# Performance work log

Hardware: AMD Instinct MI355X
Metric: run time of the kernel (lower is better)

The kernel has to match this reference:

```python
import jax, jax.numpy as jnp
import numpy as np

BLOCK = 128  # fp8 block-quant block size (block_size = [128, 128])


def _dequant(w, s):
    # w: [E, O, I] fp8-simulated values; s: [E, O, I//BLOCK] per-block scales
    # (scale_inv already repeat_interleaved along the out dim by the module).
    E, O, I = w.shape
    nb = s.shape[-1]
    bs = I // nb
    return (w.reshape(E, O, nb, bs) * s[..., None]).reshape(E, O, I)


def setup_inputs() -> dict:
    key = jax.random.key(0)
    ks = jax.random.split(key, 8)
    B, S, H, I, E = 1, 512, 2048, 768, 16
    return {
        "hidden_states": jax.random.normal(ks[0], (B, S, H), jnp.float32),
        "gate_w": jax.random.normal(ks[1], (E, H), jnp.float32) * 0.02,
        "w1": jax.random.normal(ks[2], (E, I, H), jnp.float32),
        "w1_scale": jax.random.uniform(ks[3], (E, I, H // BLOCK), jnp.float32, 0.005, 0.02),
        "w3": jax.random.normal(ks[4], (E, I, H), jnp.float32),
        "w3_scale": jax.random.uniform(ks[5], (E, I, H // BLOCK), jnp.float32, 0.005, 0.02),
        "w2": jax.random.normal(ks[6], (E, H, I), jnp.float32),
        "w2_scale": jax.random.uniform(ks[7], (E, H, I // BLOCK), jnp.float32, 0.005, 0.02),
        "top_k": 2,
    }


def reference(hidden_states, gate_w, w1, w1_scale, w3, w3_scale, w2, w2_scale, top_k):
    B, S, H = hidden_states.shape
    x = hidden_states.reshape(-1, H)           # [T, H]
    T = x.shape[0]
    E = gate_w.shape[0]

    # Router: sigmoid scores, top-k, sum-normalization (norm_topk_prob=False)
    router_logits = x @ gate_w.T               # [T, E]
    scores = jax.nn.sigmoid(router_logits.astype(jnp.float32))
    top_w, top_i = jax.lax.top_k(scores, top_k)
    top_w = top_w / jnp.sum(top_w, axis=-1, keepdims=True)

    # Dense combine matrix [T, E] (top-k sparse in the real kernel)
    combine = jnp.zeros((T, E), x.dtype).at[jnp.arange(T)[:, None], top_i].add(
        top_w.astype(x.dtype))

    # Inline block dequantization of fp8 weights
    w1d = _dequant(w1, w1_scale)               # [E, I, H]
    w3d = _dequant(w3, w3_scale)               # [E, I, H]
    w2d = _dequant(w2, w2_scale)               # [E, H, I]

    # SwiGLU expert MLPs (grouped GEMM expressed densely over experts)
    g = jnp.einsum('th,eih->eti', x, w1d)      # gate proj
    u = jnp.einsum('th,eih->eti', x, w3d)      # up proj
    a = jax.nn.silu(g) * u                     # [E, T, I]
    expert_out = jnp.einsum('eti,ehi->eth', a, w2d)  # down proj [E, T, H]

    y = jnp.einsum('te,eth->th', combine, expert_out)
    return y.reshape(B, S, H)
```

## Files before the change

kernel.cpp:

```cpp
#include <hip/hip_runtime.h>
#include <math.h>

#define H 2048
#define II 768
#define TT 512
#define EE 16
#define BK 64

typedef float f32x4 __attribute__((ext_vector_type(4)));
typedef short s16x8 __attribute__((ext_vector_type(8)));
typedef unsigned short u16;
typedef u16 u16x4 __attribute__((ext_vector_type(4)));
typedef u16 u16x8 __attribute__((ext_vector_type(8)));

__device__ __forceinline__ u16 f2bf(float f) {
  unsigned int u = __float_as_uint(f);
  u += 0x7fffu + ((u >> 16) & 1u);
  return (u16)(u >> 16);
}

__global__ void router_kernel(const float* __restrict__ x, const float* __restrict__ gw,
                              int* __restrict__ counts, int* __restrict__ topi,
                              float* __restrict__ topw, int* __restrict__ pos) {
  int t = blockIdx.x;
  int tid = threadIdx.x;
  int wave = tid >> 6, lane = tid & 63;
  __shared__ float logits[EE];
  const float* xt = x + (size_t)t * H;
  for (int e = wave * 4; e < wave * 4 + 4; ++e) {
    const float* ge = gw + (size_t)e * H;
    float p = 0.f;
    for (int h = lane * 4; h < H; h += 64 * 4) {
      f32x4 xv = *(const f32x4*)(xt + h);
      f32x4 gv = *(const f32x4*)(ge + h);
      p += xv[0]*gv[0] + xv[1]*gv[1] + xv[2]*gv[2] + xv[3]*gv[3];
    }
    #pragma unroll
    for (int off = 32; off > 0; off >>= 1) p += __shfl_down(p, off);
    if (lane == 0) logits[e] = p;
  }
  __syncthreads();
  if (tid == 0) {
    float s[EE];
    #pragma unroll
    for (int e = 0; e < EE; ++e) s[e] = 1.f / (1.f + expf(-logits[e]));
    int i0 = 0;
    for (int e = 1; e < EE; ++e) if (s[e] > s[i0]) i0 = e;
    int i1 = -1;
    for (int e = 0; e < EE; ++e) {
      if (e == i0) continue;
      if (i1 < 0 || s[e] > s[i1]) i1 = e;
    }
    float w0 = s[i0], w1v = s[i1];
    float inv = 1.f / (w0 + w1v);
    w0 *= inv; w1v *= inv;
    topi[t*2+0] = i0; topi[t*2+1] = i1;
    topw[t*2+0] = w0; topw[t*2+1] = w1v;
    pos[t*2+0] = atomicAdd(&counts[i0], 1);
    pos[t*2+1] = atomicAdd(&counts[i1], 1);
  }
}

__global__ void prefix_kernel(const int* __restrict__ counts, int* __restrict__ base) {
  int s = 0;
  for (int e = 0; e < EE; ++e) { base[e] = s; s += counts[e]; }
  base[EE] = s;
}

__global__ void gather_kernel(const float* __restrict__ x, const int* __restrict__ topi,
                              const float* __restrict__ topw, const int* __restrict__ pos,
                              const int* __restrict__ base, u16* __restrict__ Xg,
                              int* __restrict__ tok_of, float* __restrict__ wt_of) {
  int t = blockIdx.x, slot = blockIdx.y;
  int e = topi[t*2 + slot];
  int row = base[e] + pos[t*2 + slot];
  if (threadIdx.x == 0) { tok_of[row] = t; wt_of[row] = topw[t*2 + slot]; }
  const float* xt = x + (size_t)t * H;
  u16* dst = Xg + (size_t)row * H;
  int h = threadIdx.x * 8;
  f32x4 v0 = *(const f32x4*)(xt + h);
  f32x4 v1 = *(const f32x4*)(xt + h + 4);
  u16x8 o;
  o[0]=f2bf(v0[0]); o[1]=f2bf(v0[1]); o[2]=f2bf(v0[2]); o[3]=f2bf(v0[3]);
  o[4]=f2bf(v1[0]); o[5]=f2bf(v1[1]); o[6]=f2bf(v1[2]); o[7]=f2bf(v1[3]);
  *(u16x8*)(dst + h) = o;
}

__global__ __launch_bounds__(256, 8) void gemm1_kernel(
    const u16* __restrict__ Xg,
    const float* __restrict__ w1, const float* __restrict__ w1s,
    const float* __restrict__ w3, const float* __restrict__ w3s,
    const int* __restrict__ counts, const int* __restrict__ base,
    float* __restrict__ slab) {
  const int bx = blockIdx.x;
  const int nc = bx >> 2, kc = bx & 3;
  const int e = blockIdx.y;
  const int cnt = counts[e];
  if (cnt == 0) return;
  const int n0 = nc * 16;
  const int k0 = kc * 512;
  const int b0 = base[e];
  const int tid = threadIdx.x;
  const int lane = tid & 63;
  const int w = tid >> 6;

  __shared__ __align__(16) u16 As[64 * 64];
  __shared__ __align__(16) u16 Bs[2][16 * 64];

  const int rA = tid >> 3;
  const int cA = (tid & 7) << 3;
  const int cAs = cA ^ ((rA & 7) << 3);
  const int isB3 = tid >> 7;
  const int rB = (tid & 127) >> 3;
  const int cBs = cA ^ ((rB & 7) << 3);
  const float* wsrc = (isB3 ? w3 : w1) + (size_t)(e * II + n0 + rB) * H + k0 + cA;
  const float* ssrc = (isB3 ? w3s : w1s) + (size_t)(e * II + n0 + rB) * (H / 128) + kc * 4;
  u16* bdst = &Bs[isB3][rB * 64 + cBs];

  const int arow = w * 16 + (lane & 15);
  const int acol0 = (lane >> 4) << 3;
  const int brow = lane & 15;
  const int aswz = (arow & 7) << 3;
  const int bswz = (brow & 7) << 3;

  float* outG = slab + ((size_t)kc) * ((size_t)1024 * II);
  float* outU = slab + ((size_t)(4 + kc)) * ((size_t)1024 * II);

  const int nmt = (cnt + 63) >> 6;
  for (int mt = 0; mt < nmt; ++mt) {
    const u16* asrc = Xg + (size_t)(b0 + mt * 64 + rA) * H + k0 + cA;
    f32x4 accg = {}, accu = {};
    s16x8 a0, a1; f32x4 bv0, bv1; float sc;
    a0 = *(const s16x8*)(asrc);
    a1 = *(const s16x8*)(asrc + (size_t)32 * H);
    bv0 = *(const f32x4*)(wsrc);
    bv1 = *(const f32x4*)(wsrc + 4);
    sc = ssrc[0];
    {
      *(s16x8*)(As + rA * 64 + cAs) = a0;
      *(s16x8*)(As + (rA + 32) * 64 + cAs) = a1;
      u16x8 ob;
      ob[0]=f2bf(bv0[0]*sc); ob[1]=f2bf(bv0[1]*sc); ob[2]=f2bf(bv0[2]*sc); ob[3]=f2bf(bv0[3]*sc);
      ob[4]=f2bf(bv1[0]*sc); ob[5]=f2bf(bv1[1]*sc); ob[6]=f2bf(bv1[2]*sc); ob[7]=f2bf(bv1[3]*sc);
      *(u16x8*)bdst = ob;
    }
    __syncthreads();
    for (int t = 0; t < 512 / BK; ++t) {
      const bool notlast = (t + 1 < 512 / BK);
      if (notlast) {
        const int k1 = (t + 1) * BK;
        a0 = *(const s16x8*)(asrc + k1);
        a1 = *(const s16x8*)(asrc + (size_t)32 * H + k1);
        bv0 = *(const f32x4*)(wsrc + k1);
        bv1 = *(const f32x4*)(wsrc + k1 + 4);
        sc = ssrc[k1 >> 7];
      }
      #pragma unroll
      for (int ks = 0; ks < 2; ++ks) {
        const int ac = ks * 32 + acol0;
        s16x8 af  = *(const s16x8*)(As + arow * 64 + (ac ^ aswz));
        const int bix = brow * 64 + (ac ^ bswz);
        s16x8 b1f = *(const s16x8*)(Bs[0] + bix);
        s16x8 b3f = *(const s16x8*)(Bs[1] + bix);
        accg = __builtin_amdgcn_mfma_f32_16x16x32_bf16(af, b1f, accg, 0, 0, 0);
        accu = __builtin_amdgcn_mfma_f32_16x16x32_bf16(af, b3f, accu, 0, 0, 0);
      }
      __syncthreads();
      if (notlast) {
        *(s16x8*)(As + rA * 64 + cAs) = a0;
        *(s16x8*)(As + (rA + 32) * 64 + cAs) = a1;
        u16x8 ob;
        ob[0]=f2bf(bv0[0]*sc); ob[1]=f2bf(bv0[1]*sc); ob[2]=f2bf(bv0[2]*sc); ob[3]=f2bf(bv0[3]*sc);
        ob[4]=f2bf(bv1[0]*sc); ob[5]=f2bf(bv1[1]*sc); ob[6]=f2bf(bv1[2]*sc); ob[7]=f2bf(bv1[3]*sc);
        *(u16x8*)bdst = ob;
      }
      __syncthreads();
    }
    const int col = n0 + (lane & 15);
    #pragma unroll
    for (int r4 = 0; r4 < 4; ++r4) {
      int mrow = mt * 64 + w * 16 + ((lane >> 4) << 2) + r4;
      if (mrow < cnt) {
        outG[(size_t)(b0 + mrow) * II + col] = accg[r4];
        outU[(size_t)(b0 + mrow) * II + col] = accu[r4];
      }
    }
  }
}

__global__ void silu_kernel(const float* __restrict__ slab, u16* __restrict__ Ag) {
  const size_t i = ((size_t)blockIdx.x * 256 + threadIdx.x) * 4;
  const float* G = slab;
  const float* U = slab + (size_t)4 * 1024 * II;
  f32x4 g = {}, u = {};
  #pragma unroll
  for (int kc = 0; kc < 4; ++kc) {
    g += *(const f32x4*)(G + (size_t)kc * 1024 * II + i);
    u += *(const f32x4*)(U + (size_t)kc * 1024 * II + i);
  }
  u16x4 o;
  #pragma unroll
  for (int j = 0; j < 4; ++j) {
    float a = g[j] / (1.f + expf(-g[j])) * u[j];
    o[j] = f2bf(a);
  }
  *(u16x4*)(Ag + i) = o;
}

__global__ __launch_bounds__(256, 8) void gemm2_kernel(
    const u16* __restrict__ Ag,
    const float* __restrict__ w2, const float* __restrict__ w2s,
    const int* __restrict__ counts, const int* __restrict__ base,
    const int* __restrict__ tok_of, const float* __restrict__ wt_of,
    float* __restrict__ y) {
  const int bx = blockIdx.x;
  const int nc = bx >> 1, kc = bx & 1;
  const int e = blockIdx.y;
  const int cnt = counts[e];
  if (cnt == 0) return;
  const int n0 = nc * 32;
  const int k0 = kc * 384;
  const int b0 = base[e];
  const int tid = threadIdx.x;
  const int lane = tid & 63;
  const int w = tid >> 6;

  __shared__ __align__(16) u16 As[64 * 64];
  __shared__ __align__(16) u16 Bs[32 * 64];

  const int rA = tid >> 3;
  const int cA = (tid & 7) << 3;
  const int cAs = cA ^ ((rA & 7) << 3);
  const int rB = tid >> 3;
  const int cBs = cA ^ ((rB & 7) << 3);
  const float* wsrc = w2 + (size_t)(e * H + n0 + rB) * II + k0 + cA;
  const float* ssrc = w2s + (size_t)(e * H + n0 + rB) * (II / 128) + kc * 3;
  u16* bdst = &Bs[rB * 64 + cBs];

  const int arow = w * 16 + (lane & 15);
  const int acol0 = (lane >> 4) << 3;
  const int brow = lane & 15;
  const int aswz = (arow & 7) << 3;

  const int nmt = (cnt + 63) >> 6;
  for (int mt = 0; mt < nmt; ++mt) {
    const u16* asrc = Ag + (size_t)(b0 + mt * 64 + rA) * II + k0 + cA;
    f32x4 acc0 = {}, acc1 = {};
    s16x8 a0, a1; f32x4 bv0, bv1; float sc;
    a0 = *(const s16x8*)(asrc);
    a1 = *(const s16x8*)(asrc + (size_t)32 * II);
    bv0 = *(const f32x4*)(wsrc);
    bv1 = *(const f32x4*)(wsrc + 4);
    sc = ssrc[0];
    {
      *(s16x8*)(As + rA * 64 + cAs) = a0;
      *(s16x8*)(As + (rA + 32) * 64 + cAs) = a1;
      u16x8 ob;
      ob[0]=f2bf(bv0[0]*sc); ob[1]=f2bf(bv0[1]*sc); ob[2]=f2bf(bv0[2]*sc); ob[3]=f2bf(bv0[3]*sc);
      ob[4]=f2bf(bv1[0]*sc); ob[5]=f2bf(bv1[1]*sc); ob[6]=f2bf(bv1[2]*sc); ob[7]=f2bf(bv1[3]*sc);
      *(u16x8*)bdst = ob;
    }
    __syncthreads();
    for (int t = 0; t < 384 / BK; ++t) {
      const bool notlast = (t + 1 < 384 / BK);
      if (notlast) {
        const int k1 = (t + 1) * BK;
        a0 = *(const s16x8*)(asrc + k1);
        a1 = *(const s16x8*)(asrc + (size_t)32 * II + k1);
        bv0 = *(const f32x4*)(wsrc + k1);
        bv1 = *(const f32x4*)(wsrc + k1 + 4);
        sc = ssrc[k1 >> 7];
      }
      #pragma unroll
      for (int ks = 0; ks < 2; ++ks) {
        const int ac = ks * 32 + acol0;
        s16x8 af  = *(const s16x8*)(As + arow * 64 + (ac ^ aswz));
        s16x8 b0f = *(const s16x8*)(Bs + brow * 64 + (ac ^ ((brow & 7) << 3)));
        const int br1 = brow + 16;
        s16x8 b1f = *(const s16x8*)(Bs + br1 * 64 + (ac ^ ((br1 & 7) << 3)));
        acc0 = __builtin_amdgcn_mfma_f32_16x16x32_bf16(af, b0f, acc0, 0, 0, 0);
        acc1 = __builtin_amdgcn_mfma_f32_16x16x32_bf16(af, b1f, acc1, 0, 0, 0);
      }
      __syncthreads();
      if (notlast) {
        *(s16x8*)(As + rA * 64 + cAs) = a0;
        *(s16x8*)(As + (rA + 32) * 64 + cAs) = a1;
        u16x8 ob;
        ob[0]=f2bf(bv0[0]*sc); ob[1]=f2bf(bv0[1]*sc); ob[2]=f2bf(bv0[2]*sc); ob[3]=f2bf(bv0[3]*sc);
        ob[4]=f2bf(bv1[0]*sc); ob[5]=f2bf(bv1[1]*sc); ob[6]=f2bf(bv1[2]*sc); ob[7]=f2bf(bv1[3]*sc);
        *(u16x8*)bdst = ob;
      }
      __syncthreads();
    }
    #pragma unroll
    for (int r4 = 0; r4 < 4; ++r4) {
      int mrow = mt * 64 + w * 16 + ((lane >> 4) << 2) + r4;
      if (mrow < cnt) {
        int grow = b0 + mrow;
        int t = tok_of[grow];
        float wt = wt_of[grow];
        atomicAdd(y + (size_t)t * H + n0 + (lane & 15), acc0[r4] * wt);
        atomicAdd(y + (size_t)t * H + n0 + 16 + (lane & 15), acc1[r4] * wt);
      }
    }
  }
}

extern "C" void kernel_launch(void* const* d_in, const int* in_sizes, int n_in,
                              void* d_out, int out_size, void* d_ws, size_t ws_size,
                              hipStream_t stream) {
  const float* x   = (const float*)d_in[0];
  const float* gw  = (const float*)d_in[1];
  const float* w1  = (const float*)d_in[2];
  const float* w1s = (const float*)d_in[3];
  const float* w3  = (const float*)d_in[4];
  const float* w3s = (const float*)d_in[5];
  const float* w2  = (const float*)d_in[6];
  const float* w2s = (const float*)d_in[7];
  float* y = (float*)d_out;

  char* ws = (char*)d_ws;
  int*   counts = (int*)(ws + 0);
  int*   basep  = (int*)(ws + 64);
  int*   topi   = (int*)(ws + 256);
  float* topw   = (float*)(ws + 256 + 4096);
  int*   pos    = (int*)(ws + 256 + 8192);
  int*   tok_of = (int*)(ws + 256 + 12288);
  float* wt_of  = (float*)(ws + 256 + 16384);
  u16*   Xg     = (u16*)(ws + 20736);
  u16*   Ag     = (u16*)(ws + 20736 + 4718592);
  float* slab   = (float*)(ws + 20736 + 4718592 + 1769472);

  hipMemsetAsync(counts, 0, 64, stream);
  hipMemsetAsync(y, 0, (size_t)out_size * sizeof(float), stream);

  router_kernel<<<TT, 256, 0, stream>>>(x, gw, counts, topi, topw, pos);
  prefix_kernel<<<1, 1, 0, stream>>>(counts, basep);
  gather_kernel<<<dim3(TT, 2), 256, 0, stream>>>(x, topi, topw, pos, basep, Xg, tok_of, wt_of);
  gemm1_kernel<<<dim3(48 * 4, EE), 256, 0, stream>>>(Xg, w1, w1s, w3, w3s, counts, basep, slab);
  silu_kernel<<<(1024 * II) / (256 * 4), 256, 0, stream>>>(slab, Ag);
  gemm2_kernel<<<dim3(64 * 2, EE), 256, 0, stream>>>(Ag, w2, w2s, counts, basep, tok_of, wt_of, y);
}
```

Measured before the change: 139.6 us.

## Widen gemm1 N-tile to 32 with 2x2 wave layout and hoisted scales

```diff
diff --git a/kernel.cpp b/kernel.cpp
--- a/kernel.cpp
+++ b/kernel.cpp
@@ -92,36 +92,39 @@
     const float* __restrict__ w3, const float* __restrict__ w3s,
     const int* __restrict__ counts, const int* __restrict__ base,
     float* __restrict__ slab) {
-  const int bx = blockIdx.x;
-  const int nc = bx >> 2, kc = bx & 3;
+  const int nc = blockIdx.x >> 2, kc = blockIdx.x & 3;
   const int e = blockIdx.y;
   const int cnt = counts[e];
   if (cnt == 0) return;
-  const int n0 = nc * 16;
+  const int n0 = nc * 32;
   const int k0 = kc * 512;
   const int b0 = base[e];
   const int tid = threadIdx.x;
   const int lane = tid & 63;
-  const int w = tid >> 6;
+  const int wv = tid >> 6;
+  const int wm = wv >> 1, wn = wv & 1;
 
   __shared__ __align__(16) u16 As[64 * 64];
-  __shared__ __align__(16) u16 Bs[2][16 * 64];
+  __shared__ __align__(16) u16 Bs[2][32 * 64];
 
   const int rA = tid >> 3;
   const int cA = (tid & 7) << 3;
   const int cAs = cA ^ ((rA & 7) << 3);
   const int isB3 = tid >> 7;
-  const int rB = (tid & 127) >> 3;
-  const int cBs = cA ^ ((rB & 7) << 3);
-  const float* wsrc = (isB3 ? w3 : w1) + (size_t)(e * II + n0 + rB) * H + k0 + cA;
-  const float* ssrc = (isB3 ? w3s : w1s) + (size_t)(e * II + n0 + rB) * (H / 128) + kc * 4;
-  u16* bdst = &Bs[isB3][rB * 64 + cBs];
-
-  const int arow = w * 16 + (lane & 15);
-  const int acol0 = (lane >> 4) << 3;
-  const int brow = lane & 15;
-  const int aswz = (arow & 7) << 3;
-  const int bswz = (brow & 7) << 3;
+  const int rB = (tid & 127) >> 2;
+  const int cB = (tid & 3) << 4;
+  const int swzB = (rB & 7) << 3;
+  const float* wsrc = (isB3 ? w3 : w1) + ((size_t)e * II + n0 + rB) * H + k0 + cB;
+  const float* ssrc = (isB3 ? w3s : w1s) + ((size_t)e * II + n0 + rB) * (H / 128) + kc * 4;
+  float scl[4];
+  #pragma unroll
+  for (int j = 0; j < 4; ++j) scl[j] = ssrc[j];
+  u16* bdst = &Bs[isB3][rB * 64];
+
+  const int lane15 = lane & 15;
+  const int lh = lane >> 4;
+  const int brn = wn * 16 + lane15;
+  const int bswz = (brn & 7) << 3;
 
   float* outG = slab + ((size_t)kc) * ((size_t)1024 * II);
   float* outU = slab + ((size_t)(4 + kc)) * ((size_t)1024 * II);
@@ -129,20 +132,25 @@
   const int nmt = (cnt + 63) >> 6;
   for (int mt = 0; mt < nmt; ++mt) {
     const u16* asrc = Xg + (size_t)(b0 + mt * 64 + rA) * H + k0 + cA;
-    f32x4 accg = {}, accu = {};
-    s16x8 a0, a1; f32x4 bv0, bv1; float sc;
+    f32x4 accg[2] = {}, accu[2] = {};
+    s16x8 a0, a1; f32x4 bv[4]; float sc;
     a0 = *(const s16x8*)(asrc);
     a1 = *(const s16x8*)(asrc + (size_t)32 * H);
-    bv0 = *(const f32x4*)(wsrc);
-    bv1 = *(const f32x4*)(wsrc + 4);
-    sc = ssrc[0];
+    #pragma unroll
+    for (int j = 0; j < 4; ++j) bv[j] = *(const f32x4*)(wsrc + j * 4);
+    sc = scl[0];
     {
       *(s16x8*)(As + rA * 64 + cAs) = a0;
       *(s16x8*)(As + (rA + 32) * 64 + cAs) = a1;
-      u16x8 ob;
-      ob[0]=f2bf(bv0[0]*sc); ob[1]=f2bf(bv0[1]*sc); ob[2]=f2bf(bv0[2]*sc); ob[3]=f2bf(bv0[3]*sc);
-      ob[4]=f2bf(bv1[0]*sc); ob[5]=f2bf(bv1[1]*sc); ob[6]=f2bf(bv1[2]*sc); ob[7]=f2bf(bv1[3]*sc);
-      *(u16x8*)bdst = ob;
+      #pragma unroll
+      for (int j = 0; j < 2; ++j) {
+        u16x8 ob;
+        ob[0]=f2bf(bv[2*j][0]*sc); ob[1]=f2bf(bv[2*j][1]*sc);
+        ob[2]=f2bf(bv[2*j][2]*sc); ob[3]=f2bf(bv[2*j][3]*sc);
+        ob[4]=f2bf(bv[2*j+1][0]*sc); ob[5]=f2bf(bv[2*j+1][1]*sc);
+        ob[6]=f2bf(bv[2*j+1][2]*sc); ob[7]=f2bf(bv[2*j+1][3]*sc);
+        *(u16x8*)(bdst + ((cB + j * 8) ^ swzB)) = ob;
+      }
     }
     __syncthreads();
     for (int t = 0; t < 512 / BK; ++t) {
@@ -151,38 +159,49 @@
         const int k1 = (t + 1) * BK;
         a0 = *(const s16x8*)(asrc + k1);
         a1 = *(const s16x8*)(asrc + (size_t)32 * H + k1);
-        bv0 = *(const f32x4*)(wsrc + k1);
-        bv1 = *(const f32x4*)(wsrc + k1 + 4);
-        sc = ssrc[k1 >> 7];
+        #pragma unroll
+        for (int j = 0; j < 4; ++j) bv[j] = *(const f32x4*)(wsrc + k1 + j * 4);
+        sc = scl[(t + 1) >> 1];
       }
       #pragma unroll
       for (int ks = 0; ks < 2; ++ks) {
-        const int ac = ks * 32 + acol0;
-        s16x8 af  = *(const s16x8*)(As + arow * 64 + (ac ^ aswz));
-        const int bix = brow * 64 + (ac ^ bswz);
-        s16x8 b1f = *(const s16x8*)(Bs[0] + bix);
-        s16x8 b3f = *(const s16x8*)(Bs[1] + bix);
-        accg = __builtin_amdgcn_mfma_f32_16x16x32_bf16(af, b1f, accg, 0, 0, 0);
-        accu = __builtin_amdgcn_mfma_f32_16x16x32_bf16(af, b3f, accu, 0, 0, 0);
+        const int ac = ks * 32 + (lh << 3);
+        s16x8 b1f = *(const s16x8*)(Bs[0] + brn * 64 + (ac ^ bswz));
+        s16x8 b3f = *(const s16x8*)(Bs[1] + brn * 64 + (ac ^ bswz));
+        #pragma unroll
+        for (int mi = 0; mi < 2; ++mi) {
+          const int arow = wm * 32 + mi * 16 + lane15;
+          s16x8 af = *(const s16x8*)(As + arow * 64 + (ac ^ ((arow & 7) << 3)));
+          accg[mi] = __builtin_amdgcn_mfma_f32_16x16x32_bf16(af, b1f, accg[mi], 0, 0, 0);
+          accu[mi] = __builtin_amdgcn_mfma_f32_16x16x32_bf16(af, b3f, accu[mi], 0, 0, 0);
+        }
       }
       __syncthreads();
       if (notlast) {
         *(s16x8*)(As + rA * 64 + cAs) = a0;
         *(s16x8*)(As + (rA + 32) * 64 + cAs) = a1;
-        u16x8 ob;
-        ob[0]=f2bf(bv0[0]*sc); ob[1]=f2bf(bv0[1]*sc); ob[2]=f2bf(bv0[2]*sc); ob[3]=f2bf(bv0[3]*sc);
-        ob[4]=f2bf(bv1[0]*sc); ob[5]=f2bf(bv1[1]*sc); ob[6]=f2bf(bv1[2]*sc); ob[7]=f2bf(bv1[3]*sc);
-        *(u16x8*)bdst = ob;
+        #pragma unroll
+        for (int j = 0; j < 2; ++j) {
+          u16x8 ob;
+          ob[0]=f2bf(bv[2*j][0]*sc); ob[1]=f2bf(bv[2*j][1]*sc);
+          ob[2]=f2bf(bv[2*j][2]*sc); ob[3]=f2bf(bv[2*j][3]*sc);
+          ob[4]=f2bf(bv[2*j+1][0]*sc); ob[5]=f2bf(bv[2*j+1][1]*sc);
+          ob[6]=f2bf(bv[2*j+1][2]*sc); ob[7]=f2bf(bv[2*j+1][3]*sc);
+          *(u16x8*)(bdst + ((cB + j * 8) ^ swzB)) = ob;
+        }
       }
       __syncthreads();
     }
-    const int col = n0 + (lane & 15);
-    #pragma unroll
-    for (int r4 = 0; r4 < 4; ++r4) {
-      int mrow = mt * 64 + w * 16 + ((lane >> 4) << 2) + r4;
-      if (mrow < cnt) {
-        outG[(size_t)(b0 + mrow) * II + col] = accg[r4];
-        outU[(size_t)(b0 + mrow) * II + col] = accu[r4];
+    const int col = n0 + wn * 16 + lane15;
+    #pragma unroll
+    for (int mi = 0; mi < 2; ++mi) {
+      #pragma unroll
+      for (int r4 = 0; r4 < 4; ++r4) {
+        const int mrow = mt * 64 + wm * 32 + mi * 16 + (lh << 2) + r4;
+        if (mrow < cnt) {
+          outG[(size_t)(b0 + mrow) * II + col] = accg[mi][r4];
+          outU[(size_t)(b0 + mrow) * II + col] = accu[mi][r4];
+        }
       }
     }
   }
@@ -337,7 +356,7 @@
   router_kernel<<<TT, 256, 0, stream>>>(x, gw, counts, topi, topw, pos);
   prefix_kernel<<<1, 1, 0, stream>>>(counts, basep);
   gather_kernel<<<dim3(TT, 2), 256, 0, stream>>>(x, topi, topw, pos, basep, Xg, tok_of, wt_of);
-  gemm1_kernel<<<dim3(48 * 4, EE), 256, 0, stream>>>(Xg, w1, w1s, w3, w3s, counts, basep, slab);
+  gemm1_kernel<<<dim3(96, EE), 256, 0, stream>>>(Xg, w1, w1s, w3, w3s, counts, basep, slab);
   silu_kernel<<<(1024 * II) / (256 * 4), 256, 0, stream>>>(slab, Ag);
   gemm2_kernel<<<dim3(64 * 2, EE), 256, 0, stream>>>(Ag, w2, w2s, counts, basep, tok_of, wt_of, y);
 }
```

After: 167.1 us. 19.7% more time.
